# Performance work log

Hardware: AMD Instinct MI355X
Metric: run time of the kernel (lower is better)

The kernel has to match this reference:

```python
import jax, jax.numpy as jnp
import numpy as np

B, L, D, Y = 8, 2500, 512, 8921


def setup_inputs() -> dict:
    key = jax.random.key(0)
    k1, k2, k3, k4, k5 = jax.random.split(key, 5)
    x = jax.random.normal(k1, (B, L, D), dtype=jnp.float32)
    target = jax.random.uniform(k2, (B, Y), dtype=jnp.float32)
    U_w = jax.random.normal(k3, (Y, D), dtype=jnp.float32) * (1.0 / np.sqrt(D))
    final_w = jax.random.normal(k4, (Y, D), dtype=jnp.float32) * (1.0 / np.sqrt(D))
    final_b = jax.random.normal(k5, (Y,), dtype=jnp.float32) * 0.01
    return {"x": x, "target": target, "text_inputs": 0,
            "U_w": U_w, "final_w": final_w, "final_b": final_b}


def _bce_with_logits(y, t):
    # stable mean BCE-with-logits, matching torch BCEWithLogitsLoss (reduction='mean')
    return jnp.mean(jnp.maximum(y, 0.0) - y * t + jnp.log1p(jnp.exp(-jnp.abs(y))))


def reference(x, target, text_inputs, U_w, final_w, final_b):
    # label-wise attention scores: [B, Y, L]
    scores = jnp.einsum('yd,bld->byl', U_w, x)
    alpha = jax.nn.softmax(scores, axis=-1)
    # attended context per label: [B, Y, D]
    m = jnp.einsum('byl,bld->byd', alpha, x)
    # per-label dot-product readout: [B, Y]
    y = jnp.einsum('yd,byd->by', final_w, m) + final_b
    loss = _bce_with_logits(y, target)
    return (y, loss)
```

## Files before the change

kernel.cpp:

```cpp
#include <hip/hip_runtime.h>
#include <math.h>

#define B_  8
#define L_  2500
#define D_  512
#define Y_  8921
#define LP  2560
#define YP  8960

#define WS_F16_HALVES  (B_ * LP * D_ + 2 * YP * D_)
#define ACC_FLOATS     (2 * B_ * YP)

typedef _Float16 f16x8 __attribute__((ext_vector_type(8)));
typedef float    f32x4 __attribute__((ext_vector_type(4)));

__device__ __forceinline__ void load_lds16(const _Float16* g, _Float16* l) {
  __builtin_amdgcn_global_load_lds(
      (const __attribute__((address_space(1))) unsigned int*)g,
      (__attribute__((address_space(3))) unsigned int*)l, 16, 0, 0);
}

__global__ void k_convert(const float* __restrict__ x,
                          const float* __restrict__ Uw,
                          const float* __restrict__ Fw,
                          _Float16* __restrict__ ws,
                          float* __restrict__ loss_slot) {
  if (blockIdx.x == 0 && threadIdx.x == 0) *loss_slot = 0.0f;
  const int NX = B_ * LP * (D_ / 8);
  int idx = blockIdx.x * 256 + threadIdx.x;
  if (idx < ACC_FLOATS) ((float*)(ws + WS_F16_HALVES))[idx] = 0.0f;
  const float* src = nullptr;
  if (idx < NX) {
    int b  = idx / (LP * 64);
    int r  = idx - b * (LP * 64);
    int l  = r >> 6;
    int d8 = r & 63;
    if (l < L_) src = x + (((long)b * L_ + l) * D_ + d8 * 8);
  } else {
    int u    = idx - NX;
    int lane = u & 63;
    int mi   = (u >> 6) & 7;
    int kk2  = (u >> 9) & 15;
    int yt   = u >> 13;
    int grow = yt * 128 + mi * 16 + (lane & 15);
    int sub  = grow & 15;
    int y    = (grow >> 4) * 8 + (sub & 7);
    int k8   = kk2 * 4 + (lane >> 4);
    if (y < Y_) src = (sub < 8 ? Uw : Fw) + (long)y * D_ + k8 * 8;
  }
  f16x8 o;
  if (src) {
    const float4* s4 = (const float4*)src;
    float4 a = s4[0], c = s4[1];
    o[0] = (_Float16)a.x; o[1] = (_Float16)a.y; o[2] = (_Float16)a.z; o[3] = (_Float16)a.w;
    o[4] = (_Float16)c.x; o[5] = (_Float16)c.y; o[6] = (_Float16)c.z; o[7] = (_Float16)c.w;
  } else {
    for (int i = 0; i < 8; ++i) o[i] = (_Float16)0.0f;
  }
  ((f16x8*)ws)[idx] = o;
}

__global__ __launch_bounds__(256, 2)
void k_attn(const _Float16* __restrict__ ws,
            float* __restrict__ accG) {
  __shared__ __align__(16) _Float16 XT[2][16384];

  const int tid  = threadIdx.x;
  const int lane = tid & 63;
  const int wave = tid >> 6;
  const int wy = wave & 1;
  const int wl = wave >> 1;
  const int yt = blockIdx.x;
  const int b  = blockIdx.y;
  const int lh = blockIdx.z;

  const _Float16* Xg = ws + (long)b * LP * D_ + (long)lh * (LP / 2) * D_;
  const _Float16* Ga = ws + (long)B_ * LP * D_ + (long)yt * (128 * 512)
                          + (wy * 4) * 512 + lane * 8;

  const int srow = lane >> 3;
  const int sg8  = ((lane & 7) ^ srow) * 8;
  const _Float16* xbase = Xg + (long)(wave * 64 + srow) * D_ + sg8;
  _Float16* lbase = &XT[0][wave * 4096];

  const int xrow = wl * 128 + (lane & 15);
  const int r7   = lane & 7;
  const int gb   = lane >> 4;
  const bool sLow = (lane < 32);

  float redP[4][4];
  #pragma unroll
  for (int i = 0; i < 4; ++i)
    for (int v = 0; v < 4; ++v) redP[i][v] = 0.0f;

  #pragma unroll
  for (int i = 0; i < 8; ++i)
    load_lds16(xbase + i * 4096, lbase + i * 512);
  __builtin_amdgcn_sched_barrier(0);
  f16x8 au[2][4];
  #pragma unroll
  for (int ks = 0; ks < 2; ++ks)
    #pragma unroll
    for (int mi = 0; mi < 4; ++mi)
      au[ks][mi] = *(const f16x8*)(Ga + (size_t)(ks) * 4096 + mi * 512);
  __builtin_amdgcn_sched_barrier(0);
  #pragma unroll
  for (int i = 0; i < 8; ++i)
    load_lds16(xbase + 64 + i * 4096, lbase + 16384 + i * 512);
  __builtin_amdgcn_sched_barrier(0);

  for (int lt = 0; lt < 5; ++lt) {
    f32x4 acc[4][8];
    #pragma unroll
    for (int mi = 0; mi < 4; ++mi)
      for (int ni = 0; ni < 8; ++ni) {
        f32x4 z = {0.0f, 0.0f, 0.0f, 0.0f};
        acc[mi][ni] = z;
      }
    #pragma unroll 2
    for (int kk = 0; kk < 8; ++kk) {
      const int s   = lt * 8 + kk;
      const int cur = kk & 1;
      asm volatile("s_waitcnt vmcnt(16)" ::: "memory");
      __builtin_amdgcn_s_barrier();
      __builtin_amdgcn_sched_barrier(0);
      __builtin_amdgcn_s_setprio(1);
      #pragma unroll
      for (int ks = 0; ks < 2; ++ks) {
        const int off = (((ks * 4 + gb) ^ r7) * 8);
        f16x8 bx[8];
        #pragma unroll
        for (int ni = 0; ni < 8; ++ni)
          bx[ni] = *(const f16x8*)&XT[cur][(xrow + ni * 16) * 64 + off];
        #pragma unroll
        for (int mi = 0; mi < 4; ++mi)
          #pragma unroll
          for (int ni = 0; ni < 8; ++ni)
            acc[mi][ni] = __builtin_amdgcn_mfma_f32_16x16x32_f16(au[ks][mi], bx[ni], acc[mi][ni], 0, 0, 0);
      }
      __builtin_amdgcn_s_setprio(0);
      if (kk == 7) {
        #pragma unroll
        for (int mi = 0; mi < 4; ++mi)
          for (int ni = 0; ni < 8; ++ni)
            #pragma unroll
            for (int v = 0; v < 4; ++v) {
              float a = acc[mi][ni][v];
              float e = __expf(a);
              float p = __shfl_xor(e, 32, 64);
              redP[mi][v] += sLow ? e : p * a;
            }
      }
      __builtin_amdgcn_s_barrier();
      __builtin_amdgcn_sched_barrier(0);
      {
        const int kkn = (kk + 1) & 7;
        #pragma unroll
        for (int ks = 0; ks < 2; ++ks)
          #pragma unroll
          for (int mi = 0; mi < 4; ++mi)
            au[ks][mi] = *(const f16x8*)(Ga + (size_t)(kkn * 2 + ks) * 4096 + mi * 512);
      }
      __builtin_amdgcn_sched_barrier(0);
      {
        const int  sp  = (s + 2 < 40) ? s + 2 : 39;
        const long ofs = (long)(sp >> 3) * (256 * D_) + (long)(sp & 7) * 64;
        _Float16* dst = lbase + cur * 16384;
        #pragma unroll
        for (int i = 0; i < 8; ++i)
          load_lds16(xbase + ofs + i * 4096, dst + i * 512);
      }
      __builtin_amdgcn_sched_barrier(0);
    }
  }

  for (int m = 1; m < 16; m <<= 1)
    #pragma unroll
    for (int mi = 0; mi < 4; ++mi)
      for (int v = 0; v < 4; ++v)
        redP[mi][v] += __shfl_xor(redP[mi][v], m, 64);
  if ((lane & 15) == 0) {
    float* dst = accG + (sLow ? 0 : B_ * YP);
    #pragma unroll
    for (int mi = 0; mi < 4; ++mi)
      for (int v = 0; v < 4; ++v) {
        int y = yt * 64 + wy * 32 + mi * 8 + ((lane >> 4) & 1) * 4 + v;
        atomicAdd(&dst[b * YP + y], redP[mi][v]);
      }
  }
}

__global__ void k_final(const float* __restrict__ accG,
                        const float* __restrict__ fb,
                        float* __restrict__ out) {
  int id = blockIdx.x * 256 + threadIdx.x;
  if (id >= B_ * Y_) return;
  int b = id / Y_, y = id - b * Y_;
  float den = accG[b * YP + y] - (float)(LP - L_);
  out[id] = accG[B_ * YP + b * YP + y] / den + fb[y];
}

__global__ void k_loss(const float* __restrict__ y,
                       const float* __restrict__ t,
                       float* __restrict__ loss) {
  float p = 0.0f;
  for (int i = blockIdx.x * 256 + threadIdx.x; i < B_ * Y_; i += gridDim.x * 256) {
    float v = y[i], tg = t[i];
    p += fmaxf(v, 0.0f) - v * tg + log1pf(__expf(-fabsf(v)));
  }
  for (int m = 32; m; m >>= 1) p += __shfl_down(p, m, 64);
  __shared__ float wsum[4];
  int lane = threadIdx.x & 63, wv = threadIdx.x >> 6;
  if (lane == 0) wsum[wv] = p;
  __syncthreads();
  if (threadIdx.x == 0) {
    float s = wsum[0] + wsum[1] + wsum[2] + wsum[3];
    atomicAdd(loss, s * (1.0f / (float)(B_ * Y_)));
  }
}

extern "C" void kernel_launch(void* const* d_in, const int* in_sizes, int n_in,
                              void* d_out, int out_size, void* d_ws, size_t ws_size,
                              hipStream_t stream) {
  (void)in_sizes; (void)n_in; (void)out_size; (void)ws_size;
  const float* x       = (const float*)d_in[0];
  const float* target  = (const float*)d_in[1];
  const float* U_w     = (const float*)d_in[3];
  const float* final_w = (const float*)d_in[4];
  const float* final_b = (const float*)d_in[5];
  float* out = (float*)d_out;
  _Float16* ws = (_Float16*)d_ws;
  float* accG = (float*)(ws + WS_F16_HALVES);

  k_convert<<<9600, 256, 0, stream>>>(x, U_w, final_w, ws, out + B_ * Y_);

  dim3 g(YP / 64, B_, 2);
  k_attn<<<g, 256, 0, stream>>>(ws, accG);

  k_final<<<(B_ * Y_ + 255) / 256, 256, 0, stream>>>(accG, final_b, out);
  k_loss<<<140, 256, 0, stream>>>(out, target, out + B_ * Y_);
}
```

Measured before the change: 561.4 us.

## Use 512-thread blocks with triple-buffered LDS and interleaved per-quarter prefetch

The attention GEMM block grows from 4 to 8 waves covering 128 label rows, so each X tile staged in LDS is shared by twice as many label rows. LDS moves from double to triple buffering with rotating offsets. The global-to-LDS prefetch of the next tile is split into four pieces, each issued between the B-fragment reads and the MFMAs of one quarter. The aim is to halve X re-reads across blocks and to hide load latency, at the cost of a barrier per quarter, more LDS (96KB), and register pressure under 512-thread launch bounds.

```diff
diff --git a/kernel.cpp b/kernel.cpp
--- a/kernel.cpp
+++ b/kernel.cpp
@@ -60,28 +60,29 @@
   ((f16x8*)ws)[idx] = o;
 }
 
-__global__ __launch_bounds__(256, 2)
+__global__ __launch_bounds__(512, 2)
 void k_attn(const _Float16* __restrict__ ws,
             float* __restrict__ accG) {
-  __shared__ __align__(16) _Float16 XT[2][16384];
+  __shared__ __align__(16) _Float16 XT[49152];
 
   const int tid  = threadIdx.x;
   const int lane = tid & 63;
   const int wave = tid >> 6;
-  const int wy = wave & 1;
-  const int wl = wave >> 1;
+  const int wy = wave >> 1;
+  const int wl = wave & 1;
   const int yt = blockIdx.x;
   const int b  = blockIdx.y;
   const int lh = blockIdx.z;
 
   const _Float16* Xg = ws + (long)b * LP * D_ + (long)lh * (LP / 2) * D_;
-  const _Float16* Ga = ws + (long)B_ * LP * D_ + (long)yt * (128 * 512)
-                          + (wy * 4) * 512 + lane * 8;
+  const _Float16* Ga = ws + (long)B_ * LP * D_
+                          + (long)(yt * 2 + (wy >> 1)) * (128 * 512)
+                          + (wy & 1) * (4 * 512) + lane * 8;
 
   const int srow = lane >> 3;
   const int sg8  = ((lane & 7) ^ srow) * 8;
-  const _Float16* xbase = Xg + (long)(wave * 64 + srow) * D_ + sg8;
-  _Float16* lbase = &XT[0][wave * 4096];
+  const _Float16* xbase = Xg + (long)(wave * 32 + srow) * D_ + sg8;
+  const int ldst = wave * 2048;
 
   const int xrow = wl * 128 + (lane & 15);
   const int r7   = lane & 7;
@@ -93,22 +94,28 @@
   for (int i = 0; i < 4; ++i)
     for (int v = 0; v < 4; ++v) redP[i][v] = 0.0f;
 
-  #pragma unroll
-  for (int i = 0; i < 8; ++i)
-    load_lds16(xbase + i * 4096, lbase + i * 512);
+  int ofR = 0, of1 = 16384, ofW = 32768;
+
+  #pragma unroll
+  for (int i = 0; i < 4; ++i)
+    load_lds16(xbase + i * 4096, XT + 0 + ldst + i * 512);
+  __builtin_amdgcn_sched_barrier(0);
+  #pragma unroll
+  for (int i = 0; i < 4; ++i)
+    load_lds16(xbase + 64 + i * 4096, XT + 16384 + ldst + i * 512);
   __builtin_amdgcn_sched_barrier(0);
   f16x8 au[2][4];
   #pragma unroll
   for (int ks = 0; ks < 2; ++ks)
     #pragma unroll
     for (int mi = 0; mi < 4; ++mi)
-      au[ks][mi] = *(const f16x8*)(Ga + (size_t)(ks) * 4096 + mi * 512);
-  __builtin_amdgcn_sched_barrier(0);
-  #pragma unroll
-  for (int i = 0; i < 8; ++i)
-    load_lds16(xbase + 64 + i * 4096, lbase + 16384 + i * 512);
-  __builtin_amdgcn_sched_barrier(0);
-
+      au[ks][mi] = *(const f16x8*)(Ga + (size_t)ks * 4096 + mi * 512);
+  __builtin_amdgcn_sched_barrier(0);
+  asm volatile("s_waitcnt vmcnt(8)" ::: "memory");
+  __builtin_amdgcn_s_barrier();
+  __builtin_amdgcn_sched_barrier(0);
+
+  #pragma unroll 1
   for (int lt = 0; lt < 5; ++lt) {
     f32x4 acc[4][8];
     #pragma unroll
@@ -117,60 +124,64 @@
         f32x4 z = {0.0f, 0.0f, 0.0f, 0.0f};
         acc[mi][ni] = z;
       }
-    #pragma unroll 2
+    #pragma unroll 1
     for (int kk = 0; kk < 8; ++kk) {
       const int s   = lt * 8 + kk;
-      const int cur = kk & 1;
-      asm volatile("s_waitcnt vmcnt(16)" ::: "memory");
-      __builtin_amdgcn_s_barrier();
-      __builtin_amdgcn_sched_barrier(0);
-      __builtin_amdgcn_s_setprio(1);
+      const int kkn = (kk + 1) & 7;
+      const int sp  = (s + 2 < 40) ? s + 2 : 39;
+      const long ofs_next = (long)(sp >> 3) * (256 * D_) + (long)(sp & 7) * 64;
       #pragma unroll
-      for (int ks = 0; ks < 2; ++ks) {
-        const int off = (((ks * 4 + gb) ^ r7) * 8);
-        f16x8 bx[8];
+      for (int q = 0; q < 4; ++q) {
+        f16x8 bq[2][2];
         #pragma unroll
-        for (int ni = 0; ni < 8; ++ni)
-          bx[ni] = *(const f16x8*)&XT[cur][(xrow + ni * 16) * 64 + off];
-        #pragma unroll
-        for (int mi = 0; mi < 4; ++mi)
+        for (int ks = 0; ks < 2; ++ks)
           #pragma unroll
-          for (int ni = 0; ni < 8; ++ni)
-            acc[mi][ni] = __builtin_amdgcn_mfma_f32_16x16x32_f16(au[ks][mi], bx[ni], acc[mi][ni], 0, 0, 0);
-      }
-      __builtin_amdgcn_s_setprio(0);
-      if (kk == 7) {
-        #pragma unroll
-        for (int mi = 0; mi < 4; ++mi)
-          for (int ni = 0; ni < 8; ++ni)
-            #pragma unroll
-            for (int v = 0; v < 4; ++v) {
-              float a = acc[mi][ni][v];
-              float e = __expf(a);
-              float p = __shfl_xor(e, 32, 64);
-              redP[mi][v] += sLow ? e : p * a;
-            }
-      }
-      __builtin_amdgcn_s_barrier();
-      __builtin_amdgcn_sched_barrier(0);
-      {
-        const int kkn = (kk + 1) & 7;
+          for (int j = 0; j < 2; ++j)
+            bq[ks][j] = *(const f16x8*)&XT[ofR + (xrow + (2 * q + j) * 16) * 64
+                                           + (((ks * 4 + gb) ^ r7) * 8)];
+        __builtin_amdgcn_sched_barrier(0);
+        load_lds16(xbase + ofs_next + q * 4096, XT + ofW + ldst + q * 512);
+        __builtin_amdgcn_sched_barrier(0);
+        __builtin_amdgcn_s_barrier();
+        if (q == 0)
+          asm volatile("s_waitcnt vmcnt(1) lgkmcnt(0)" ::: "memory");
+        else
+          asm volatile("s_waitcnt lgkmcnt(0)" ::: "memory");
+        __builtin_amdgcn_sched_barrier(0);
+        __builtin_amdgcn_s_setprio(1);
         #pragma unroll
         for (int ks = 0; ks < 2; ++ks)
           #pragma unroll
           for (int mi = 0; mi < 4; ++mi)
-            au[ks][mi] = *(const f16x8*)(Ga + (size_t)(kkn * 2 + ks) * 4096 + mi * 512);
+            #pragma unroll
+            for (int j = 0; j < 2; ++j)
+              acc[mi][2 * q + j] = __builtin_amdgcn_mfma_f32_16x16x32_f16(
+                  au[ks][mi], bq[ks][j], acc[mi][2 * q + j], 0, 0, 0);
+        __builtin_amdgcn_s_setprio(0);
+        __builtin_amdgcn_sched_barrier(0);
+        if (q == 3) {
+          if (kk == 7) {
+            #pragma unroll
+            for (int mi = 0; mi < 4; ++mi)
+              for (int ni = 0; ni < 8; ++ni)
+                #pragma unroll
+                for (int v = 0; v < 4; ++v) {
+                  float a = acc[mi][ni][v];
+                  float e = __expf(a);
+                  float p = __shfl_xor(e, 32, 64);
+                  redP[mi][v] += sLow ? e : p * a;
+                }
+          }
+          #pragma unroll
+          for (int ks = 0; ks < 2; ++ks)
+            #pragma unroll
+            for (int mi = 0; mi < 4; ++mi)
+              au[ks][mi] = *(const f16x8*)(Ga + (size_t)(kkn * 2 + ks) * 4096 + mi * 512);
+          __builtin_amdgcn_sched_barrier(0);
+          __builtin_amdgcn_s_barrier();
+          int t = ofR; ofR = of1; of1 = ofW; ofW = t;
+        }
       }
-      __builtin_amdgcn_sched_barrier(0);
-      {
-        const int  sp  = (s + 2 < 40) ? s + 2 : 39;
-        const long ofs = (long)(sp >> 3) * (256 * D_) + (long)(sp & 7) * 64;
-        _Float16* dst = lbase + cur * 16384;
-        #pragma unroll
-        for (int i = 0; i < 8; ++i)
-          load_lds16(xbase + ofs + i * 4096, dst + i * 512);
-      }
-      __builtin_amdgcn_sched_barrier(0);
     }
   }
 
@@ -184,7 +195,7 @@
     #pragma unroll
     for (int mi = 0; mi < 4; ++mi)
       for (int v = 0; v < 4; ++v) {
-        int y = yt * 64 + wy * 32 + mi * 8 + ((lane >> 4) & 1) * 4 + v;
+        int y = yt * 128 + wy * 32 + mi * 8 + ((lane >> 4) & 1) * 4 + v;
         atomicAdd(&dst[b * YP + y], redP[mi][v]);
       }
   }
@@ -234,8 +245,8 @@
 
   k_convert<<<9600, 256, 0, stream>>>(x, U_w, final_w, ws, out + B_ * Y_);
 
-  dim3 g(YP / 64, B_, 2);
-  k_attn<<<g, 256, 0, stream>>>(ws, accG);
+  dim3 g(YP / 128, B_, 2);
+  k_attn<<<g, 512, 0, stream>>>(ws, accG);
 
   k_final<<<(B_ * Y_ + 255) / 256, 256, 0, stream>>>(accG, final_b, out);
   k_loss<<<140, 256, 0, stream>>>(out, target, out + B_ * Y_);
```

New measurement: 564.8 us. Within noise of the previous version (+0.6%).
